# Optimization experiments

Hardware: AMD Instinct MI355X
Metric: run time of the kernel (lower is better)

The kernel has to match this reference:

```python
import jax, jax.numpy as jnp
import numpy as np

EMBED_DIM = 256
NUM_HEADS = 8
HEAD_DIM = EMBED_DIM // NUM_HEADS
CPB_HIDDEN = 64


def setup_inputs() -> dict:
    key = jax.random.key(0)
    ks = jax.random.split(key, 12)
    B, Q, K = 4, 900, 1024
    s = 0.02
    return {
        "nodes": jax.random.normal(ks[0], (B, Q, EMBED_DIM), jnp.float32),
        "images_data": jax.random.normal(ks[1], (B, K, EMBED_DIM), jnp.float32),
        "images_mask": jnp.zeros((B, K), dtype=bool),
        "relative_distances": jax.random.normal(ks[2], (B, Q, K, 2), jnp.float32),
        "Wq": jax.random.normal(ks[3], (EMBED_DIM, EMBED_DIM), jnp.float32) * s,
        "bq": jnp.zeros((EMBED_DIM,), jnp.float32),
        "Wkv": jax.random.normal(ks[4], (2 * EMBED_DIM, EMBED_DIM), jnp.float32) * s,
        "bkv": jnp.zeros((2 * EMBED_DIM,), jnp.float32),
        "Wc1": jax.random.normal(ks[5], (CPB_HIDDEN, 2), jnp.float32) * 0.5,
        "bc1": jnp.zeros((CPB_HIDDEN,), jnp.float32),
        "Wc2": jax.random.normal(ks[6], (NUM_HEADS, CPB_HIDDEN), jnp.float32) * 0.1,
        "bc2": jnp.zeros((NUM_HEADS,), jnp.float32),
        "Wo": jax.random.normal(ks[7], (EMBED_DIM, EMBED_DIM), jnp.float32) * s,
        "bo": jnp.zeros((EMBED_DIM,), jnp.float32),
    }


def reference(nodes, images_data, images_mask, relative_distances,
              Wq, bq, Wkv, bkv, Wc1, bc1, Wc2, bc2, Wo, bo):
    B, Q, K, _ = relative_distances.shape
    H, D = NUM_HEADS, HEAD_DIM

    # query / key / value projections
    q = nodes @ Wq.T + bq                       # [B, Q, E]
    q = q.reshape(B, Q, H, D).transpose(0, 2, 1, 3)  # [B, H, Q, D]
    kv = images_data @ Wkv.T + bkv              # [B, K, 2E]
    kv = kv.reshape(B, K, 2, H, D).transpose(2, 0, 3, 1, 4)  # [2, B, H, K, D]
    k, v = kv[0], kv[1]

    # continuous position bias MLP: [B,Q,K,2] -> [B,Q,K,H]
    h = jax.nn.relu(relative_distances @ Wc1.T + bc1)
    cpb = h @ Wc2.T + bc2                       # [B, Q, K, H]
    cpb = cpb.transpose(0, 3, 1, 2)             # [B, H, Q, K]

    # mask out padded image positions
    att_mask = jnp.where(images_mask[:, None, None, :], -jnp.inf, cpb)

    # scaled dot-product attention with additive mask
    scale = 1.0 / jnp.sqrt(jnp.asarray(D, q.dtype))
    scores = jnp.einsum("bhqd,bhkd->bhqk", q, k) * scale + att_mask
    attn = jax.nn.softmax(scores, axis=-1)
    out = jnp.einsum("bhqk,bhkd->bhqd", attn, v)  # [B, H, Q, D]

    out = out.transpose(0, 2, 1, 3).reshape(B, Q, H * D)
    return out @ Wo.T + bo
```

## Files before the change

### kernel.cpp

```cpp
#include <hip/hip_runtime.h>
#include <hip/hip_bf16.h>

typedef float f32x4 __attribute__((ext_vector_type(4)));
typedef short short8 __attribute__((ext_vector_type(8)));

static __device__ __forceinline__ short f2bf(float x) {
  union { __hip_bfloat16 b; short s; } u;
  u.b = __float2bfloat16(x);
  return u.s;
}

static __device__ __forceinline__ short8 cvt8(const float* __restrict__ p) {
  const float4 lo = *(const float4*)p;
  const float4 hi = *(const float4*)(p + 4);
  short8 v;
  v[0] = f2bf(lo.x); v[1] = f2bf(lo.y); v[2] = f2bf(lo.z); v[3] = f2bf(lo.w);
  v[4] = f2bf(hi.x); v[5] = f2bf(hi.y); v[6] = f2bf(hi.z); v[7] = f2bf(hi.w);
  return v;
}

__global__ __launch_bounds__(256, 4)
void gemm_qkv_mfma(const float* __restrict__ nodes, const float* __restrict__ Wq,
                   const float* __restrict__ bq, short* __restrict__ qb,
                   const float* __restrict__ images, const float* __restrict__ Wkv,
                   const float* __restrict__ bkv, short* __restrict__ kb,
                   short* __restrict__ vT) {
  const int t = threadIdx.x, w = t >> 6, lane = t & 63;
  const int fr = lane & 15, fk = lane >> 4;
  int bid = blockIdx.x;
  const float *A, *W, *bias; int M, m0, n0, kvmode;
  if (bid < 228) {
    A = nodes; W = Wq; bias = bq; M = 3600; kvmode = 0;
    m0 = (bid >> 2) * 64; n0 = (bid & 3) * 64;
  } else {
    bid -= 228;
    A = images; W = Wkv; bias = bkv; M = 4096; kvmode = 1;
    m0 = (bid >> 3) * 64; n0 = (bid & 7) * 64;
  }
  int arow = m0 + w * 16 + fr; if (arow > M - 1) arow = M - 1;
  f32x4 acc[4];
  #pragma unroll
  for (int s = 0; s < 4; ++s) acc[s] = (f32x4){0.f, 0.f, 0.f, 0.f};
  #pragma unroll 2
  for (int k0 = 0; k0 < 256; k0 += 32) {
    const short8 af = cvt8(&A[(size_t)arow * 256 + k0 + fk * 8]);
    #pragma unroll
    for (int s = 0; s < 4; ++s) {
      const short8 wf = cvt8(&W[(size_t)(n0 + s * 16 + fr) * 256 + k0 + fk * 8]);
      acc[s] = __builtin_amdgcn_mfma_f32_16x16x32_bf16(af, wf, acc[s], 0, 0, 0);
    }
  }
  #pragma unroll
  for (int s = 0; s < 4; ++s)
    #pragma unroll
    for (int r = 0; r < 4; ++r) {
      const int m = m0 + w * 16 + fk * 4 + r;
      const int n = n0 + s * 16 + fr;
      const float val = acc[s][r] + bias[n];
      if (kvmode == 0) {
        if (m < 3600) qb[(size_t)m * 256 + n] = f2bf(val);
      } else {
        if (n < 256)
          kb[(size_t)m * 256 + n] = f2bf(val);
        else
          vT[((size_t)(m >> 10) * 256 + (n - 256)) * 1024 + (m & 1023)] =
              f2bf(val);
      }
    }
}

__global__ __launch_bounds__(256, 4)
void gemm_out_mfma(const short* __restrict__ ob, const float* __restrict__ Wo,
                   const float* __restrict__ bo, float* __restrict__ out) {
  const int t = threadIdx.x, w = t >> 6, lane = t & 63;
  const int fr = lane & 15, fk = lane >> 4;
  const int m0 = (blockIdx.x >> 2) * 64, n0 = (blockIdx.x & 3) * 64;
  int arow = m0 + w * 16 + fr; if (arow > 3599) arow = 3599;
  f32x4 acc[4];
  #pragma unroll
  for (int s = 0; s < 4; ++s) acc[s] = (f32x4){0.f, 0.f, 0.f, 0.f};
  #pragma unroll 2
  for (int k0 = 0; k0 < 256; k0 += 32) {
    const short8 af = *(const short8*)&ob[(size_t)arow * 256 + k0 + fk * 8];
    #pragma unroll
    for (int s = 0; s < 4; ++s) {
      const short8 wf = cvt8(&Wo[(size_t)(n0 + s * 16 + fr) * 256 + k0 + fk * 8]);
      acc[s] = __builtin_amdgcn_mfma_f32_16x16x32_bf16(af, wf, acc[s], 0, 0, 0);
    }
  }
  #pragma unroll
  for (int s = 0; s < 4; ++s)
    #pragma unroll
    for (int r = 0; r < 4; ++r) {
      const int m = m0 + w * 16 + fk * 4 + r;
      const int n = n0 + s * 16 + fr;
      if (m < 3600) out[(size_t)m * 256 + n] = acc[s][r] + bo[n];
    }
}

#define SCALE 0.17677669529663687f

#define BAR()                                              \
  asm volatile("s_waitcnt lgkmcnt(0)" ::: "memory");       \
  __builtin_amdgcn_s_barrier();                            \
  asm volatile("" ::: "memory")

template <int KLEN>
__global__ __launch_bounds__(512, 2)
void attn_part(const __hip_bfloat16* __restrict__ qb,
               const __hip_bfloat16* __restrict__ kb,
               const __hip_bfloat16* __restrict__ vT,
               const float* __restrict__ dist,
               const unsigned char* __restrict__ mask,
               const float* __restrict__ Wc1, const float* __restrict__ bc1,
               const float* __restrict__ Wc2, const float* __restrict__ bc2,
               float* __restrict__ Opart,
               float* __restrict__ msplit,
               float* __restrict__ lsplit) {
  constexpr int NCH = KLEN / 32;
  __shared__ float cpb_s[2][8 * 552];
  __shared__ short ps_s[8][640];

  const int t    = threadIdx.x;
  const int b    = blockIdx.x / 57;
  const int q0   = (blockIdx.x % 57) * 16;
  const int sp   = blockIdx.y;
  const int kb0  = sp * KLEN;
  const int w    = t >> 6;
  const int lane = t & 63;
  const int fr   = lane & 15;
  const int fk   = lane >> 4;

  float w1x[2][8], w1y[2][8], w1b[2][8];
  #pragma unroll
  for (int m = 0; m < 2; ++m)
    #pragma unroll
    for (int jj = 0; jj < 8; ++jj) {
      const int j = m * 32 + fk * 8 + jj;
      w1x[m][jj] = Wc1[2 * j];
      w1y[m][jj] = Wc1[2 * j + 1];
      w1b[m][jj] = bc1[j];
    }
  short8 w2f[2];
  #pragma unroll
  for (int m = 0; m < 2; ++m)
    #pragma unroll
    for (int jj = 0; jj < 8; ++jj) {
      const float v = (fr < 8) ? Wc2[fr * 64 + m * 32 + fk * 8 + jj] : 0.f;
      w2f[m][jj] = f2bf(v);
    }
  const float b2add = (fr < 8) ? bc2[fr] : 0.f;

  int qrow = q0 + fr; if (qrow > 899) qrow = 899;
  const short8 aq = *(const short8*)&qb[(size_t)(b * 900 + qrow) * 256 +
                                        w * 32 + fk * 8];

  const float* dptr[4];
  float2 d2cur[4];
  #pragma unroll
  for (int t4 = 0; t4 < 4; ++t4) {
    int qg = q0 + 2 * w + (t4 >> 1); if (qg > 899) qg = 899;
    dptr[t4] = dist +
        ((size_t)(b * 900 + qg) * 1024 + kb0 + (t4 & 1) * 16 + fr) * 2;
    d2cur[t4] = *(const float2*)dptr[t4];
  }

  f32x4 of[2];
  of[0] = (f32x4){0.f, 0.f, 0.f, 0.f};
  of[1] = (f32x4){0.f, 0.f, 0.f, 0.f};
  float mreg[4], lreg[4];
  #pragma unroll
  for (int r = 0; r < 4; ++r) { mreg[r] = -1e30f; lreg[r] = 0.f; }

  for (int c = 0; c < NCH; ++c) {
    const int k0 = kb0 + c * 32;
    const int cn = (c < NCH - 1) ? c + 1 : c;
    float* cpb_c = cpb_s[c & 1];

    float2 d2n[4];
    #pragma unroll
    for (int t4 = 0; t4 < 4; ++t4)
      d2n[t4] = *(const float2*)(dptr[t4] + (size_t)cn * 64);
    const short8 kf0 = *(const short8*)
        &kb[(size_t)(b * 1024 + k0 + fr) * 256 + w * 32 + fk * 8];
    const short8 kf1 = *(const short8*)
        &kb[(size_t)(b * 1024 + k0 + 16 + fr) * 256 + w * 32 + fk * 8];
    const short8 bv0 = *(const short8*)
        &vT[(size_t)(b * 256 + w * 32 + fr) * 1024 + k0 + fk * 8];
    const short8 bv1 = *(const short8*)
        &vT[(size_t)(b * 256 + w * 32 + 16 + fr) * 1024 + k0 + fk * 8];
    const bool mk0 = mask[b * 1024 + k0 + fr] != 0;
    const bool mk1 = mask[b * 1024 + k0 + 16 + fr] != 0;

    #pragma unroll
    for (int t4 = 0; t4 < 4; ++t4) {
      const float dx = d2cur[t4].x, dy = d2cur[t4].y;
      short8 a0, a1;
      #pragma unroll
      for (int jj = 0; jj < 8; ++jj) {
        const float h0 =
            fmaxf(fmaf(w1x[0][jj], dx, fmaf(w1y[0][jj], dy, w1b[0][jj])), 0.f);
        const float h1 =
            fmaxf(fmaf(w1x[1][jj], dx, fmaf(w1y[1][jj], dy, w1b[1][jj])), 0.f);
        a0[jj] = f2bf(h0);
        a1[jj] = f2bf(h1);
      }
      f32x4 z = {0.f, 0.f, 0.f, 0.f};
      f32x4 dcp = __builtin_amdgcn_mfma_f32_16x16x32_bf16(a1, w2f[1], z, 0, 0, 0);
      dcp = __builtin_amdgcn_mfma_f32_16x16x32_bf16(a0, w2f[0], dcp, 0, 0, 0);
      const int qloc = 2 * w + (t4 >> 1);
      const int kbase = (t4 & 1) * 16;
      if (fr < 8) {
        #pragma unroll
        for (int rr = 0; rr < 4; ++rr)
          cpb_c[fr * 552 + qloc * 34 + kbase + fk * 4 + rr] = dcp[rr] + b2add;
      }
      __builtin_amdgcn_sched_barrier(0);
    }

    BAR();

    f32x4 z = {0.f, 0.f, 0.f, 0.f};
    __builtin_amdgcn_s_setprio(1);
    const f32x4 sc0 = __builtin_amdgcn_mfma_f32_16x16x32_bf16(aq, kf0, z, 0, 0, 0);
    const f32x4 sc1 = __builtin_amdgcn_mfma_f32_16x16x32_bf16(aq, kf1, z, 0, 0, 0);
    __builtin_amdgcn_s_setprio(0);

    float s0v[4], s1v[4];
    bool need = false;
    #pragma unroll
    for (int r = 0; r < 4; ++r) {
      const int q = fk * 4 + r;
      const float cv0 = cpb_c[w * 552 + q * 34 + fr];
      const float cv1 = cpb_c[w * 552 + q * 34 + 16 + fr];
      s0v[r] = mk0 ? -1e30f : fmaf(sc0[r], SCALE, cv0);
      s1v[r] = mk1 ? -1e30f : fmaf(sc1[r], SCALE, cv1);
      need = need || (fmaxf(s0v[r], s1v[r]) > mreg[r] + 8.f);
    }
    if (__any((int)need)) {
      #pragma unroll
      for (int r = 0; r < 4; ++r) {
        float mx = fmaxf(s0v[r], s1v[r]);
        mx = fmaxf(mx, __shfl_xor(mx, 1));
        mx = fmaxf(mx, __shfl_xor(mx, 2));
        mx = fmaxf(mx, __shfl_xor(mx, 4));
        mx = fmaxf(mx, __shfl_xor(mx, 8));
        const float mnew = fmaxf(mreg[r], mx);
        const float al = __expf(mreg[r] - mnew);
        of[0][r] *= al;
        of[1][r] *= al;
        lreg[r] *= al;
        mreg[r] = mnew;
      }
    }
    #pragma unroll
    for (int r = 0; r < 4; ++r) {
      const int q = fk * 4 + r;
      const float p0 = __expf(s0v[r] - mreg[r]);
      const float p1 = __expf(s1v[r] - mreg[r]);
      ps_s[w][q * 40 + fr]      = f2bf(p0);
      ps_s[w][q * 40 + 16 + fr] = f2bf(p1);
      lreg[r] += p0 + p1;
    }

    asm volatile("s_waitcnt lgkmcnt(0)" ::: "memory");
    __builtin_amdgcn_sched_barrier(0);

    const short8 ap = *(const short8*)&ps_s[w][fr * 40 + fk * 8];
    __builtin_amdgcn_s_setprio(1);
    of[0] = __builtin_amdgcn_mfma_f32_16x16x32_bf16(ap, bv0, of[0], 0, 0, 0);
    of[1] = __builtin_amdgcn_mfma_f32_16x16x32_bf16(ap, bv1, of[1], 0, 0, 0);
    __builtin_amdgcn_s_setprio(0);

    #pragma unroll
    for (int t4 = 0; t4 < 4; ++t4) d2cur[t4] = d2n[t4];
  }

  #pragma unroll
  for (int r = 0; r < 4; ++r) {
    lreg[r] += __shfl_xor(lreg[r], 1);
    lreg[r] += __shfl_xor(lreg[r], 2);
    lreg[r] += __shfl_xor(lreg[r], 4);
    lreg[r] += __shfl_xor(lreg[r], 8);
  }

  #pragma unroll
  for (int s = 0; s < 2; ++s)
    #pragma unroll
    for (int r = 0; r < 4; ++r) {
      const int qg = q0 + fk * 4 + r;
      Opart[((size_t)sp * 3648 + b * 912 + qg) * 256 + w * 32 + s * 16 + fr] =
          of[s][r];
    }
  if (fr == 0) {
    #pragma unroll
    for (int r = 0; r < 4; ++r) {
      const int qg = q0 + fk * 4 + r;
      msplit[((sp * 4 + b) * 8 + w) * 912 + qg] = mreg[r];
      lsplit[((sp * 4 + b) * 8 + w) * 912 + qg] = lreg[r];
    }
  }
}

template <int NS>
__global__ __launch_bounds__(256)
void attn_combine(const float* __restrict__ Opart,
                  const float* __restrict__ msplit,
                  const float* __restrict__ lsplit,
                  short* __restrict__ obuf) {
  const int row = blockIdx.x;
  const int b = row / 900, q = row - b * 900;
  const int e = threadIdx.x, h = e >> 5;
  float mv[NS], M = -1e30f;
  #pragma unroll
  for (int s = 0; s < NS; ++s) {
    mv[s] = msplit[((s * 4 + b) * 8 + h) * 912 + q];
    M = fmaxf(M, mv[s]);
  }
  float L = 0.f, val = 0.f;
  #pragma unroll
  for (int s = 0; s < NS; ++s) {
    const float wgt = __expf(mv[s] - M);
    L = fmaf(lsplit[((s * 4 + b) * 8 + h) * 912 + q], wgt, L);
    val = fmaf(Opart[((size_t)s * 3648 + b * 912 + q) * 256 + e], wgt, val);
  }
  obuf[(size_t)row * 256 + e] = f2bf(val / L);
}

extern "C" void kernel_launch(void* const* d_in, const int* in_sizes, int n_in,
                              void* d_out, int out_size, void* d_ws, size_t ws_size,
                              hipStream_t stream) {
  const float* nodes  = (const float*)d_in[0];
  const float* images = (const float*)d_in[1];
  const unsigned char* mask = (const unsigned char*)d_in[2];
  const float* dist   = (const float*)d_in[3];
  const float* Wq     = (const float*)d_in[4];
  const float* bq     = (const float*)d_in[5];
  const float* Wkv    = (const float*)d_in[6];
  const float* bkv    = (const float*)d_in[7];
  const float* Wc1    = (const float*)d_in[8];
  const float* bc1    = (const float*)d_in[9];
  const float* Wc2    = (const float*)d_in[10];
  const float* bc2    = (const float*)d_in[11];
  const float* Wo     = (const float*)d_in[12];
  const float* bo     = (const float*)d_in[13];
  float* out = (float*)d_out;

  char* wp = (char*)d_ws;
  short* qb = (short*)wp;
  short* kb = (short*)(wp + 1843200);
  short* vT = (short*)(wp + 3940352);
  char*  S  = wp + 6037504;
  float* Opart = (float*)S;

  const size_t need2 = 6037504u + 2u * 3735552u + 2u * 2u * 116736u;
  int nsplit = (ws_size >= need2) ? 2 : 1;
  float* msplit = Opart + (size_t)nsplit * 3648 * 256;
  float* lsplit = msplit + (size_t)nsplit * 4 * 8 * 912;
  short* obuf_bf = qb;

  gemm_qkv_mfma<<<740, 256, 0, stream>>>(nodes, Wq, bq, qb,
                                         images, Wkv, bkv, kb, vT);

  if (nsplit == 2) {
    attn_part<512><<<dim3(228, 2), 512, 0, stream>>>(
        (const __hip_bfloat16*)qb, (const __hip_bfloat16*)kb,
        (const __hip_bfloat16*)vT, dist, mask, Wc1, bc1, Wc2, bc2,
        Opart, msplit, lsplit);
    attn_combine<2><<<3600, 256, 0, stream>>>(Opart, msplit, lsplit, obuf_bf);
  } else {
    attn_part<1024><<<dim3(228, 1), 512, 0, stream>>>(
        (const __hip_bfloat16*)qb, (const __hip_bfloat16*)kb,
        (const __hip_bfloat16*)vT, dist, mask, Wc1, bc1, Wc2, bc2,
        Opart, msplit, lsplit);
    attn_combine<1><<<3600, 256, 0, stream>>>(Opart, msplit, lsplit, obuf_bf);
  }

  gemm_out_mfma<<<228, 256, 0, stream>>>(obuf_bf, Wo, bo, out);
}
```

Before: 126.8 us.

## Software-pipeline CPB MLP one chunk ahead and add 4-way K split

Result: slower. 138.7 us (+9.4%).

```diff
diff --git a/kernel.cpp b/kernel.cpp
--- a/kernel.cpp
+++ b/kernel.cpp
@@ -105,6 +105,33 @@
   __builtin_amdgcn_s_barrier();                            \
   asm volatile("" ::: "memory")
 
+#define MLP_TILES(D2, CPB)                                                    \
+  _Pragma("unroll")                                                           \
+  for (int t4 = 0; t4 < 4; ++t4) {                                            \
+    const float dx = (D2)[t4].x, dy = (D2)[t4].y;                             \
+    short8 a0, a1;                                                            \
+    _Pragma("unroll")                                                         \
+    for (int jj = 0; jj < 8; ++jj) {                                          \
+      const float h0 =                                                        \
+          fmaxf(fmaf(w1x[0][jj], dx, fmaf(w1y[0][jj], dy, w1b[0][jj])), 0.f); \
+      const float h1 =                                                        \
+          fmaxf(fmaf(w1x[1][jj], dx, fmaf(w1y[1][jj], dy, w1b[1][jj])), 0.f); \
+      a0[jj] = f2bf(h0);                                                      \
+      a1[jj] = f2bf(h1);                                                      \
+    }                                                                         \
+    f32x4 zm = {0.f, 0.f, 0.f, 0.f};                                          \
+    f32x4 dcp = __builtin_amdgcn_mfma_f32_16x16x32_bf16(a1, w2f[1], zm, 0, 0, 0); \
+    dcp = __builtin_amdgcn_mfma_f32_16x16x32_bf16(a0, w2f[0], dcp, 0, 0, 0);  \
+    const int qloc = 2 * w + (t4 >> 1);                                       \
+    const int kbase = (t4 & 1) * 16;                                          \
+    if (fr < 8) {                                                             \
+      _Pragma("unroll")                                                       \
+      for (int rr = 0; rr < 4; ++rr)                                          \
+        (CPB)[fr * 552 + qloc * 34 + kbase + fk * 4 + rr] = dcp[rr] + b2add;  \
+    }                                                                         \
+    __builtin_amdgcn_sched_barrier(0);                                        \
+  }
+
 template <int KLEN>
 __global__ __launch_bounds__(512, 2)
 void attn_part(const __hip_bfloat16* __restrict__ qb,
@@ -156,13 +183,11 @@
                                         w * 32 + fk * 8];
 
   const float* dptr[4];
-  float2 d2cur[4];
   #pragma unroll
   for (int t4 = 0; t4 < 4; ++t4) {
     int qg = q0 + 2 * w + (t4 >> 1); if (qg > 899) qg = 899;
     dptr[t4] = dist +
         ((size_t)(b * 900 + qg) * 1024 + kb0 + (t4 & 1) * 16 + fr) * 2;
-    d2cur[t4] = *(const float2*)dptr[t4];
   }
 
   f32x4 of[2];
@@ -172,53 +197,33 @@
   #pragma unroll
   for (int r = 0; r < 4; ++r) { mreg[r] = -1e30f; lreg[r] = 0.f; }
 
+  float2 d2now[4];
+  {
+    float2 d2c0[4];
+    #pragma unroll
+    for (int t4 = 0; t4 < 4; ++t4) d2c0[t4] = *(const float2*)dptr[t4];
+    MLP_TILES(d2c0, cpb_s[0])
+    const int c1 = (NCH > 1) ? 1 : 0;
+    #pragma unroll
+    for (int t4 = 0; t4 < 4; ++t4)
+      d2now[t4] = *(const float2*)(dptr[t4] + (size_t)c1 * 64);
+  }
+  short8 kf0 = *(const short8*)
+      &kb[(size_t)(b * 1024 + kb0 + fr) * 256 + w * 32 + fk * 8];
+  short8 kf1 = *(const short8*)
+      &kb[(size_t)(b * 1024 + kb0 + 16 + fr) * 256 + w * 32 + fk * 8];
+  short8 bv0 = *(const short8*)
+      &vT[(size_t)(b * 256 + w * 32 + fr) * 1024 + kb0 + fk * 8];
+  short8 bv1 = *(const short8*)
+      &vT[(size_t)(b * 256 + w * 32 + 16 + fr) * 1024 + kb0 + fk * 8];
+  bool mk0 = mask[b * 1024 + kb0 + fr] != 0;
+  bool mk1 = mask[b * 1024 + kb0 + 16 + fr] != 0;
+
+  BAR();
+
   for (int c = 0; c < NCH; ++c) {
-    const int k0 = kb0 + c * 32;
-    const int cn = (c < NCH - 1) ? c + 1 : c;
-    float* cpb_c = cpb_s[c & 1];
-
-    float2 d2n[4];
-    #pragma unroll
-    for (int t4 = 0; t4 < 4; ++t4)
-      d2n[t4] = *(const float2*)(dptr[t4] + (size_t)cn * 64);
-    const short8 kf0 = *(const short8*)
-        &kb[(size_t)(b * 1024 + k0 + fr) * 256 + w * 32 + fk * 8];
-    const short8 kf1 = *(const short8*)
-        &kb[(size_t)(b * 1024 + k0 + 16 + fr) * 256 + w * 32 + fk * 8];
-    const short8 bv0 = *(const short8*)
-        &vT[(size_t)(b * 256 + w * 32 + fr) * 1024 + k0 + fk * 8];
-    const short8 bv1 = *(const short8*)
-        &vT[(size_t)(b * 256 + w * 32 + 16 + fr) * 1024 + k0 + fk * 8];
-    const bool mk0 = mask[b * 1024 + k0 + fr] != 0;
-    const bool mk1 = mask[b * 1024 + k0 + 16 + fr] != 0;
-
-    #pragma unroll
-    for (int t4 = 0; t4 < 4; ++t4) {
-      const float dx = d2cur[t4].x, dy = d2cur[t4].y;
-      short8 a0, a1;
-      #pragma unroll
-      for (int jj = 0; jj < 8; ++jj) {
-        const float h0 =
-            fmaxf(fmaf(w1x[0][jj], dx, fmaf(w1y[0][jj], dy, w1b[0][jj])), 0.f);
-        const float h1 =
-            fmaxf(fmaf(w1x[1][jj], dx, fmaf(w1y[1][jj], dy, w1b[1][jj])), 0.f);
-        a0[jj] = f2bf(h0);
-        a1[jj] = f2bf(h1);
-      }
-      f32x4 z = {0.f, 0.f, 0.f, 0.f};
-      f32x4 dcp = __builtin_amdgcn_mfma_f32_16x16x32_bf16(a1, w2f[1], z, 0, 0, 0);
-      dcp = __builtin_amdgcn_mfma_f32_16x16x32_bf16(a0, w2f[0], dcp, 0, 0, 0);
-      const int qloc = 2 * w + (t4 >> 1);
-      const int kbase = (t4 & 1) * 16;
-      if (fr < 8) {
-        #pragma unroll
-        for (int rr = 0; rr < 4; ++rr)
-          cpb_c[fr * 552 + qloc * 34 + kbase + fk * 4 + rr] = dcp[rr] + b2add;
-      }
-      __builtin_amdgcn_sched_barrier(0);
-    }
-
-    BAR();
+    const float* cpb_c = cpb_s[c & 1];
+    float* cpb_n = cpb_s[(c + 1) & 1];
 
     f32x4 z = {0.f, 0.f, 0.f, 0.f};
     __builtin_amdgcn_s_setprio(1);
@@ -263,17 +268,47 @@
       lreg[r] += p0 + p1;
     }
 
+    short8 kf0n = kf0, kf1n = kf1, bv0n = bv0, bv1n = bv1;
+    bool mk0n = mk0, mk1n = mk1;
+    if (c + 1 < NCH) {
+      const int k1 = kb0 + (c + 1) * 32;
+      kf0n = *(const short8*)
+          &kb[(size_t)(b * 1024 + k1 + fr) * 256 + w * 32 + fk * 8];
+      kf1n = *(const short8*)
+          &kb[(size_t)(b * 1024 + k1 + 16 + fr) * 256 + w * 32 + fk * 8];
+      bv0n = *(const short8*)
+          &vT[(size_t)(b * 256 + w * 32 + fr) * 1024 + k1 + fk * 8];
+      bv1n = *(const short8*)
+          &vT[(size_t)(b * 256 + w * 32 + 16 + fr) * 1024 + k1 + fk * 8];
+      mk0n = mask[b * 1024 + k1 + fr] != 0;
+      mk1n = mask[b * 1024 + k1 + 16 + fr] != 0;
+    }
+    float2 d2nx[4];
+    {
+      const int cn2 = (c + 2 < NCH) ? c + 2 : NCH - 1;
+      #pragma unroll
+      for (int t4 = 0; t4 < 4; ++t4)
+        d2nx[t4] = *(const float2*)(dptr[t4] + (size_t)cn2 * 64);
+    }
+
+    if (c + 1 < NCH) {
+      MLP_TILES(d2now, cpb_n)
+    }
+
     asm volatile("s_waitcnt lgkmcnt(0)" ::: "memory");
     __builtin_amdgcn_sched_barrier(0);
-
     const short8 ap = *(const short8*)&ps_s[w][fr * 40 + fk * 8];
     __builtin_amdgcn_s_setprio(1);
     of[0] = __builtin_amdgcn_mfma_f32_16x16x32_bf16(ap, bv0, of[0], 0, 0, 0);
     of[1] = __builtin_amdgcn_mfma_f32_16x16x32_bf16(ap, bv1, of[1], 0, 0, 0);
     __builtin_amdgcn_s_setprio(0);
 
-    #pragma unroll
-    for (int t4 = 0; t4 < 4; ++t4) d2cur[t4] = d2n[t4];
+    kf0 = kf0n; kf1 = kf1n; bv0 = bv0n; bv1 = bv1n;
+    mk0 = mk0n; mk1 = mk1n;
+    #pragma unroll
+    for (int t4 = 0; t4 < 4; ++t4) d2now[t4] = d2nx[t4];
+
+    BAR();
   }
 
   #pragma unroll
@@ -353,8 +388,11 @@
   char*  S  = wp + 6037504;
   float* Opart = (float*)S;
 
+  const size_t need4 = 6037504u + 4u * 3735552u + 4u * 2u * 116736u;
   const size_t need2 = 6037504u + 2u * 3735552u + 2u * 2u * 116736u;
-  int nsplit = (ws_size >= need2) ? 2 : 1;
+  int nsplit = 1;
+  if (ws_size >= need4) nsplit = 4;
+  else if (ws_size >= need2) nsplit = 2;
   float* msplit = Opart + (size_t)nsplit * 3648 * 256;
   float* lsplit = msplit + (size_t)nsplit * 4 * 8 * 912;
   short* obuf_bf = qb;
@@ -362,7 +400,13 @@
   gemm_qkv_mfma<<<740, 256, 0, stream>>>(nodes, Wq, bq, qb,
                                          images, Wkv, bkv, kb, vT);
 
-  if (nsplit == 2) {
+  if (nsplit == 4) {
+    attn_part<256><<<dim3(228, 4), 512, 0, stream>>>(
+        (const __hip_bfloat16*)qb, (const __hip_bfloat16*)kb,
+        (const __hip_bfloat16*)vT, dist, mask, Wc1, bc1, Wc2, bc2,
+        Opart, msplit, lsplit);
+    attn_combine<4><<<3600, 256, 0, stream>>>(Opart, msplit, lsplit, obuf_bf);
+  } else if (nsplit == 2) {
     attn_part<512><<<dim3(228, 2), 512, 0, stream>>>(
         (const __hip_bfloat16*)qb, (const __hip_bfloat16*)kb,
         (const __hip_bfloat16*)vT, dist, mask, Wc1, bc1, Wc2, bc2,
```
